# Performance work log

Measured on AMD Instinct MI355X. Metric: run time of the kernel, lower is better.

The kernel has to match this reference:

```python
import jax, jax.numpy as jnp
import numpy as np

B, N, D, H = 32, 128, 64, 128


def setup_inputs() -> dict:
    key = jax.random.key(0)
    ks = jax.random.split(key, 16)
    s = 0.05
    inp = {
        "x": jax.random.normal(ks[0], (B, N, D), dtype=jnp.float32),
        "masks": jax.random.randint(ks[1], (B, N), 0, 2, dtype=jnp.int32),
        # message_net: Linear(2D,H) -> ReLU -> Linear(H,H)
        "W1": jax.random.normal(ks[2], (2 * D, H), dtype=jnp.float32) * s,
        "b1": jax.random.normal(ks[3], (H,), dtype=jnp.float32) * s,
        "W2": jax.random.normal(ks[4], (H, H), dtype=jnp.float32) * s,
        "b2": jax.random.normal(ks[5], (H,), dtype=jnp.float32) * s,
        # attention_net: Linear(2D,H) -> ReLU -> Linear(H,1)
        "A1": jax.random.normal(ks[6], (2 * D, H), dtype=jnp.float32) * s,
        "ab1": jax.random.normal(ks[7], (H,), dtype=jnp.float32) * s,
        "A2": jax.random.normal(ks[8], (H, 1), dtype=jnp.float32) * s,
        "ab2": jax.random.normal(ks[9], (1,), dtype=jnp.float32) * s,
        # update_net: Linear(D+H,H) -> ReLU -> Linear(H,D)
        "U1": jax.random.normal(ks[10], (D + H, H), dtype=jnp.float32) * s,
        "ub1": jax.random.normal(ks[11], (H,), dtype=jnp.float32) * s,
        "U2": jax.random.normal(ks[12], (H, D), dtype=jnp.float32) * s,
        "ub2": jax.random.normal(ks[13], (D,), dtype=jnp.float32) * s,
    }
    return inp


def reference(x, masks, W1, b1, W2, b2, A1, ab1, A2, ab2, U1, ub1, U2, ub2):
    d = x.shape[-1]
    # pairs = cat([x_i, x_j]); Linear(pairs) == x_i @ W[:d] + x_j @ W[d:] + b
    # message MLP hidden: (B, N, N, H)
    h = jax.nn.relu(
        jnp.einsum("bid,dh->bih", x, W1[:d])[:, :, None, :]
        + jnp.einsum("bjd,dh->bjh", x, W1[d:])[:, None, :, :]
        + b1
    )
    messages = jnp.einsum("bijh,hk->bijk", h, W2) + b2  # (B, N, N, H)
    # attention MLP
    ha = jax.nn.relu(
        jnp.einsum("bid,dh->bih", x, A1[:d])[:, :, None, :]
        + jnp.einsum("bjd,dh->bjh", x, A1[d:])[:, None, :, :]
        + ab1
    )
    logits = jnp.einsum("bijh,h->bij", ha, A2[:, 0]) + ab2[0]  # (B, N, N)
    m = masks.astype(bool)[:, None, :]  # mask over j (source agents)
    logits = jnp.where(m, logits, -jnp.inf)
    attn = jax.nn.softmax(logits, axis=-1)
    attn = jnp.where(m, attn, 0.0)
    agg = jnp.einsum("bijh,bij->bih", messages, attn)  # (B, N, H)
    comb = jnp.concatenate([x, agg], axis=-1)  # (B, N, D+H)
    upd = jax.nn.relu(comb @ U1 + ub1) @ U2 + ub2  # (B, N, D)
    return x + upd
```

## Files before the change

### kernel.cpp

```cpp
#include <hip/hip_runtime.h>
#include <hip/hip_bf16.h>
#include <stdint.h>

#define NN 128
#define DD 64
#define HH 128

__device__ __forceinline__ float bflo(uint32_t u){ union{uint32_t u;float f;} c; c.u = u<<16; return c.f; }
__device__ __forceinline__ float bfhi(uint32_t u){ union{uint32_t u;float f;} c; c.u = u & 0xffff0000u; return c.f; }
__device__ __forceinline__ uint32_t packbf(float lo, float hi){
  __hip_bfloat16 a = __float2bfloat16(lo);
  __hip_bfloat16 b = __float2bfloat16(hi);
  uint16_t ua = *(uint16_t*)&a, ub = *(uint16_t*)&b;
  return (uint32_t)ua | ((uint32_t)ub<<16);
}

__global__ __launch_bounds__(128) void k1_proj(
    const float* __restrict__ x,
    const float* __restrict__ W1, const float* __restrict__ b1,
    const float* __restrict__ A1, const float* __restrict__ ab1,
    const float* __restrict__ W2, const float* __restrict__ b2,
    const float* __restrict__ U1, const float* __restrict__ ub1,
    float* __restrict__ Pm, float* __restrict__ Pa,
    uint32_t* __restrict__ Qmp, uint32_t* __restrict__ Qap,
    float* __restrict__ M, float* __restrict__ c0){
  const int bid = blockIdx.x;
  const int t = threadIdx.x;
  if(bid >= 512){
    int hb = bid - 512;
    if(hb < HH){
      float acc = 0.f;
      #pragma unroll 4
      for(int k=0;k<HH;k++) acc += W2[hb*HH+k] * U1[(DD+k)*HH+t];
      M[hb*HH+t] = acc;
    } else {
      float acc = ub1[t];
      #pragma unroll 4
      for(int k=0;k<HH;k++) acc += b2[k] * U1[(DD+k)*HH+t];
      c0[t] = acc;
    }
    return;
  }
  const int g = bid & 15, b = bid >> 4;
  const int jb = g*4;
  __shared__ float xs[8][64];
  __shared__ float qmS[8][128];
  __shared__ float qaS[8][128];
  {
    int r = t >> 4, d4 = (t & 15)*4;
    int gr = (r<4) ? (jb+r) : (jb + r - 4 + 64);
    *(float4*)&xs[r][d4] = *(const float4*)&x[(b*NN+gr)*DD + d4];
  }
  __syncthreads();
  float pm[8], qm[8], pa[8], qa[8];
  #pragma unroll
  for(int r=0;r<8;r++){ pm[r]=0.f;qm[r]=0.f;pa[r]=0.f;qa[r]=0.f; }
  for(int d0=0; d0<DD; d0+=4){
    float4 xr[8];
    #pragma unroll
    for(int r=0;r<8;r++) xr[r] = *(const float4*)&xs[r][d0];
    #pragma unroll
    for(int dd=0; dd<4; dd++){
      const int d = d0 + dd;
      float w1a = W1[d*HH + t];
      float w1b = W1[(DD+d)*HH + t];
      float a1a = A1[d*HH + t];
      float a1b = A1[(DD+d)*HH + t];
      #pragma unroll
      for(int r=0;r<8;r++){
        float xv = (&xr[r].x)[dd];
        pm[r] += xv*w1a; qm[r] += xv*w1b;
        pa[r] += xv*a1a; qa[r] += xv*a1b;
      }
    }
  }
  float b1v = b1[t], ab1v = ab1[t];
  #pragma unroll
  for(int r=0;r<8;r++){
    int gr = (r<4) ? (jb+r) : (jb + r - 4 + 64);
    Pm[(b*NN+gr)*HH + t] = pm[r] + b1v;
    Pa[(b*NN+gr)*HH + t] = pa[r] + ab1v;
    qmS[r][t] = qm[r];
    qaS[r][t] = qa[r];
  }
  __syncthreads();
  #pragma unroll
  for(int k=0;k<4;k++){
    int idx = t + k*128;
    int r = idx >> 6, hp = idx & 63;
    int gr = (r<4) ? (jb+r) : (jb + r - 4 + 64);
    Qmp[(b*NN+gr)*64 + hp] = packbf(qmS[r][hp], qmS[r][hp+64]);
    Qap[(b*NN+gr)*64 + hp] = packbf(qaS[r][hp], qaS[r][hp+64]);
  }
}

__global__ __launch_bounds__(256) void k2_fused(
    const float* __restrict__ Pa, const float* __restrict__ Pm,
    const uint32_t* __restrict__ Qap, const uint32_t* __restrict__ Qmp,
    const float* __restrict__ A2, const int* __restrict__ masks,
    const float* __restrict__ x, const float* __restrict__ M,
    const float* __restrict__ c0,
    const float* __restrict__ U1, const float* __restrict__ U2,
    const float* __restrict__ ub2, float* __restrict__ out){
  const int it = blockIdx.x;
  const int b  = blockIdx.y;
  const int t = threadIdx.x;
  const int wave = t>>6, lane = t&63;
  __shared__ uint32_t qbuf[NN*65];
  __shared__ float pS[8*HH];
  __shared__ float a2S[HH];
  __shared__ float atS[8*NN];
  __shared__ float xs[8][DD];
  {
    const uint32_t* src = Qap + (size_t)b*NN*64;
    #pragma unroll
    for(int k=0;k<8;k++){
      int idx4 = t + k*256;
      int j = idx4 >> 4, hp4 = (idx4 & 15)*4;
      uint4 v = *(const uint4*)&src[j*64 + hp4];
      uint32_t* d = &qbuf[j*65 + hp4];
      d[0]=v.x; d[1]=v.y; d[2]=v.z; d[3]=v.w;
    }
    int r = t>>5, h4 = (t&31)*4;
    *(float4*)&pS[r*HH + h4] = *(const float4*)&Pa[(b*NN + it*8 + r)*HH + h4];
    if(t < HH) a2S[t] = A2[t];
    if(t < 128){
      int xr = t >> 4, d4 = (t & 15)*4;
      *(float4*)&xs[xr][d4] = *(const float4*)&x[(b*NN + it*8 + xr)*DD + d4];
    }
  }
  __syncthreads();
  const int i0 = wave*2, i1 = i0+1;
  float a00=0.f,a01=0.f,a10=0.f,a11=0.f;
  for(int h0=0; h0<64; h0+=4){
    float4 p0a = *(const float4*)&pS[i0*HH + h0];
    float4 p0b = *(const float4*)&pS[i0*HH + 64 + h0];
    float4 p1a = *(const float4*)&pS[i1*HH + h0];
    float4 p1b = *(const float4*)&pS[i1*HH + 64 + h0];
    float4 a2a = *(const float4*)&a2S[h0];
    float4 a2b = *(const float4*)&a2S[64 + h0];
    #pragma unroll
    for(int dd=0; dd<4; dd++){
      uint32_t q0 = qbuf[lane*65 + h0 + dd];
      uint32_t q1 = qbuf[(lane+64)*65 + h0 + dd];
      float q0l=bflo(q0), q0h=bfhi(q0), q1l=bflo(q1), q1h=bfhi(q1);
      float pa0=(&p0a.x)[dd], pb0=(&p0b.x)[dd];
      float pa1=(&p1a.x)[dd], pb1=(&p1b.x)[dd];
      float aa=(&a2a.x)[dd],  ab=(&a2b.x)[dd];
      a00 += fmaxf(pa0+q0l,0.f)*aa; a00 += fmaxf(pb0+q0h,0.f)*ab;
      a01 += fmaxf(pa0+q1l,0.f)*aa; a01 += fmaxf(pb0+q1h,0.f)*ab;
      a10 += fmaxf(pa1+q0l,0.f)*aa; a10 += fmaxf(pb1+q0h,0.f)*ab;
      a11 += fmaxf(pa1+q1l,0.f)*aa; a11 += fmaxf(pb1+q1h,0.f)*ab;
    }
  }
  const int m0 = masks[b*NN + lane];
  const int m1 = masks[b*NN + 64 + lane];
  const float NEG = -3.0e38f;
  #pragma unroll
  for(int ii=0; ii<2; ii++){
    float x0 = ii ? a10 : a00, x1 = ii ? a11 : a01;
    int il = ii ? i1 : i0;
    float l0 = m0 ? x0 : NEG, l1 = m1 ? x1 : NEG;
    float v = fmaxf(l0, l1);
    for(int off=32; off>=1; off>>=1) v = fmaxf(v, __shfl_xor(v, off));
    float e0 = m0 ? __expf(x0 - v) : 0.f;
    float e1 = m1 ? __expf(x1 - v) : 0.f;
    float s = e0 + e1;
    for(int off=32; off>=1; off>>=1) s += __shfl_xor(s, off);
    float inv = (s > 0.f) ? (1.f/s) : 0.f;
    atS[il*NN + lane]      = e0*inv;
    atS[il*NN + 64 + lane] = e1*inv;
  }
  __syncthreads();
  {
    const uint32_t* src = Qmp + (size_t)b*NN*64;
    #pragma unroll
    for(int k=0;k<8;k++){
      int idx4 = t + k*256;
      int j = idx4 >> 4, hp4 = (idx4 & 15)*4;
      uint4 v = *(const uint4*)&src[j*64 + hp4];
      uint32_t* d = &qbuf[j*65 + hp4];
      d[0]=v.x; d[1]=v.y; d[2]=v.z; d[3]=v.w;
    }
    int r = t>>5, h4 = (t&31)*4;
    *(float4*)&pS[r*HH + h4] = *(const float4*)&Pm[(b*NN + it*8 + r)*HH + h4];
  }
  __syncthreads();
  float pm00 = pS[i0*HH + lane], pm01 = pS[i0*HH + 64 + lane];
  float pm10 = pS[i1*HH + lane], pm11 = pS[i1*HH + 64 + lane];
  float h00=0.f,h01=0.f,h10=0.f,h11=0.f;
  for(int j0=0; j0<NN; j0+=4){
    float4 at0 = *(const float4*)&atS[i0*NN + j0];
    float4 at1 = *(const float4*)&atS[i1*NN + j0];
    #pragma unroll
    for(int dd=0; dd<4; dd++){
      uint32_t qd = qbuf[(j0+dd)*65 + lane];
      float ql = bflo(qd), qh = bfhi(qd);
      float w0 = (&at0.x)[dd], w1 = (&at1.x)[dd];
      h00 += w0*fmaxf(pm00+ql,0.f);
      h01 += w0*fmaxf(pm01+qh,0.f);
      h10 += w1*fmaxf(pm10+ql,0.f);
      h11 += w1*fmaxf(pm11+qh,0.f);
    }
  }
  __syncthreads();
  pS[i0*HH + lane]      = h00;
  pS[i0*HH + 64 + lane] = h01;
  pS[i1*HH + lane]      = h10;
  pS[i1*HH + 64 + lane] = h11;
  __syncthreads();
  {
    const int c = t & 127, gg = t >> 7;
    float acc[4];
    #pragma unroll
    for(int r=0;r<4;r++) acc[r]=0.f;
    for(int d0=0; d0<DD; d0+=4){
      float u0 = U1[(d0+0)*HH + c];
      float u1 = U1[(d0+1)*HH + c];
      float u2 = U1[(d0+2)*HH + c];
      float u3 = U1[(d0+3)*HH + c];
      #pragma unroll
      for(int r=0;r<4;r++){
        float4 xv = *(const float4*)&xs[gg*4+r][d0];
        acc[r] += xv.x*u0 + xv.y*u1 + xv.z*u2 + xv.w*u3;
      }
    }
    for(int h0=0; h0<HH; h0+=4){
      float m0v = M[(h0+0)*HH + c];
      float m1v = M[(h0+1)*HH + c];
      float m2v = M[(h0+2)*HH + c];
      float m3v = M[(h0+3)*HH + c];
      #pragma unroll
      for(int r=0;r<4;r++){
        float4 hv = *(const float4*)&pS[(gg*4+r)*HH + h0];
        acc[r] += hv.x*m0v + hv.y*m1v + hv.z*m2v + hv.w*m3v;
      }
    }
    float cc = c0[c];
    #pragma unroll
    for(int r=0;r<4;r++) atS[(gg*4+r)*NN + c] = fmaxf(acc[r]+cc, 0.f);
  }
  __syncthreads();
  {
    const int dcol = t & 63, rg = t >> 6;
    float acc2[2];
    acc2[0]=0.f; acc2[1]=0.f;
    for(int ci=0; ci<HH; ci+=4){
      float u20 = U2[(ci+0)*DD + dcol];
      float u21 = U2[(ci+1)*DD + dcol];
      float u22 = U2[(ci+2)*DD + dcol];
      float u23 = U2[(ci+3)*DD + dcol];
      #pragma unroll
      for(int r=0;r<2;r++){
        float4 hv = *(const float4*)&atS[(rg*2+r)*NN + ci];
        acc2[r] += hv.x*u20 + hv.y*u21 + hv.z*u22 + hv.w*u23;
      }
    }
    float ub = ub2[dcol];
    #pragma unroll
    for(int r=0;r<2;r++){
      int grow = b*NN + it*8 + rg*2 + r;
      out[grow*DD + dcol] = xs[rg*2+r][dcol] + acc2[r] + ub;
    }
  }
}

extern "C" void kernel_launch(void* const* d_in, const int* in_sizes, int n_in,
                              void* d_out, int out_size, void* d_ws, size_t ws_size,
                              hipStream_t stream){
  const float* x   = (const float*)d_in[0];
  const int*   msk = (const int*)d_in[1];
  const float* W1  = (const float*)d_in[2];
  const float* b1  = (const float*)d_in[3];
  const float* W2  = (const float*)d_in[4];
  const float* b2  = (const float*)d_in[5];
  const float* A1  = (const float*)d_in[6];
  const float* ab1 = (const float*)d_in[7];
  const float* A2  = (const float*)d_in[8];
  const float* U1  = (const float*)d_in[10];
  const float* ub1 = (const float*)d_in[11];
  const float* U2  = (const float*)d_in[12];
  const float* ub2 = (const float*)d_in[13];
  float* out = (float*)d_out;

  char* w = (char*)d_ws;
  float*    Pm   = (float*)(w);
  float*    Pa   = (float*)(w + (2u<<20));
  uint32_t* Qmp  = (uint32_t*)(w + (4u<<20));
  uint32_t* Qap  = (uint32_t*)(w + (5u<<20));
  float*    M    = (float*)(w + (8u<<20));
  float*    c0   = (float*)(w + (8u<<20) + (64u<<10));

  hipLaunchKernelGGL(k1_proj, dim3(641), dim3(128), 0, stream,
                     x, W1, b1, A1, ab1, W2, b2, U1, ub1,
                     Pm, Pa, Qmp, Qap, M, c0);
  hipLaunchKernelGGL(k2_fused, dim3(16,32), dim3(256), 0, stream,
                     Pa, Pm, Qap, Qmp, A2, msk, x, M, c0, U1, U2, ub2, out);
}
```

Measured before the change: 117.1 us.

## Compact unmasked source agents and skip masked columns in fused attention kernel

Builds a compacted list of unmasked source indices per batch with a ballot and prefix popcount, then loads only those rows of the projected Q tensors into shared memory. The attention-logit loop skips the upper 64-column half when fewer than 64 sources remain, and the aggregation loop runs only over the compacted count. Masked sources get zero attention weight in the reference, so this removes work on them without changing the result. In exchange it adds two extra block barriers and some index bookkeeping, and the saving depends on the mask density (about half the agents are masked in the test inputs).

Measured after the change: 116.4 us. About the same (-0.6%).

```diff
diff --git a/kernel.cpp b/kernel.cpp
--- a/kernel.cpp
+++ b/kernel.cpp
@@ -111,16 +111,15 @@
   __shared__ float a2S[HH];
   __shared__ float atS[8*NN];
   __shared__ float xs[8][DD];
-  {
-    const uint32_t* src = Qap + (size_t)b*NN*64;
-    #pragma unroll
-    for(int k=0;k<8;k++){
-      int idx4 = t + k*256;
-      int j = idx4 >> 4, hp4 = (idx4 & 15)*4;
-      uint4 v = *(const uint4*)&src[j*64 + hp4];
-      uint32_t* d = &qbuf[j*65 + hp4];
-      d[0]=v.x; d[1]=v.y; d[2]=v.z; d[3]=v.w;
-    }
+  __shared__ unsigned long long balS[2];
+  __shared__ int jlS[NN];
+  int mym = 0;
+  if(t < 128) mym = masks[b*NN + t];
+  {
+    unsigned long long bal = __ballot(mym != 0);
+    if(wave < 2 && lane == 0) balS[wave] = bal;
+  }
+  {
     int r = t>>5, h4 = (t&31)*4;
     *(float4*)&pS[r*HH + h4] = *(const float4*)&Pa[(b*NN + it*8 + r)*HH + h4];
     if(t < HH) a2S[t] = A2[t];
@@ -130,7 +129,28 @@
     }
   }
   __syncthreads();
+  const int cnt0 = __popcll(balS[0]);
+  const int cnt  = cnt0 + __popcll(balS[1]);
+  const int cnt4 = (cnt + 3) & ~3;
+  if(t < 128 && mym){
+    unsigned long long bw = balS[wave];
+    int pos = __popcll(bw & ((1ull<<lane)-1)) + (wave ? cnt0 : 0);
+    jlS[pos] = t;
+  }
+  __syncthreads();
+  {
+    const uint32_t* src = Qap + (size_t)b*NN*64;
+    for(int idx4 = t; idx4 < cnt4*16; idx4 += 256){
+      int j = idx4 >> 4, hp4 = (idx4 & 15)*4;
+      uint4 v = make_uint4(0u,0u,0u,0u);
+      if(j < cnt) v = *(const uint4*)&src[jlS[j]*64 + hp4];
+      uint32_t* d = &qbuf[j*65 + hp4];
+      d[0]=v.x; d[1]=v.y; d[2]=v.z; d[3]=v.w;
+    }
+  }
+  __syncthreads();
   const int i0 = wave*2, i1 = i0+1;
+  const bool hasHi = (cnt > 64);
   float a00=0.f,a01=0.f,a10=0.f,a11=0.f;
   for(int h0=0; h0<64; h0+=4){
     float4 p0a = *(const float4*)&pS[i0*HH + h0];
@@ -142,29 +162,38 @@
     #pragma unroll
     for(int dd=0; dd<4; dd++){
       uint32_t q0 = qbuf[lane*65 + h0 + dd];
-      uint32_t q1 = qbuf[(lane+64)*65 + h0 + dd];
-      float q0l=bflo(q0), q0h=bfhi(q0), q1l=bflo(q1), q1h=bfhi(q1);
+      float q0l=bflo(q0), q0h=bfhi(q0);
       float pa0=(&p0a.x)[dd], pb0=(&p0b.x)[dd];
       float pa1=(&p1a.x)[dd], pb1=(&p1b.x)[dd];
       float aa=(&a2a.x)[dd],  ab=(&a2b.x)[dd];
       a00 += fmaxf(pa0+q0l,0.f)*aa; a00 += fmaxf(pb0+q0h,0.f)*ab;
-      a01 += fmaxf(pa0+q1l,0.f)*aa; a01 += fmaxf(pb0+q1h,0.f)*ab;
       a10 += fmaxf(pa1+q0l,0.f)*aa; a10 += fmaxf(pb1+q0h,0.f)*ab;
-      a11 += fmaxf(pa1+q1l,0.f)*aa; a11 += fmaxf(pb1+q1h,0.f)*ab;
-    }
-  }
-  const int m0 = masks[b*NN + lane];
-  const int m1 = masks[b*NN + 64 + lane];
+    }
+    if(hasHi){
+      #pragma unroll
+      for(int dd=0; dd<4; dd++){
+        uint32_t q1 = qbuf[(lane+64)*65 + h0 + dd];
+        float q1l=bflo(q1), q1h=bfhi(q1);
+        float pa0=(&p0a.x)[dd], pb0=(&p0b.x)[dd];
+        float pa1=(&p1a.x)[dd], pb1=(&p1b.x)[dd];
+        float aa=(&a2a.x)[dd],  ab=(&a2b.x)[dd];
+        a01 += fmaxf(pa0+q1l,0.f)*aa; a01 += fmaxf(pb0+q1h,0.f)*ab;
+        a11 += fmaxf(pa1+q1l,0.f)*aa; a11 += fmaxf(pb1+q1h,0.f)*ab;
+      }
+    }
+  }
+  const bool v0c = (lane < cnt);
+  const bool v1c = (lane + 64 < cnt);
   const float NEG = -3.0e38f;
   #pragma unroll
   for(int ii=0; ii<2; ii++){
     float x0 = ii ? a10 : a00, x1 = ii ? a11 : a01;
     int il = ii ? i1 : i0;
-    float l0 = m0 ? x0 : NEG, l1 = m1 ? x1 : NEG;
+    float l0 = v0c ? x0 : NEG, l1 = v1c ? x1 : NEG;
     float v = fmaxf(l0, l1);
     for(int off=32; off>=1; off>>=1) v = fmaxf(v, __shfl_xor(v, off));
-    float e0 = m0 ? __expf(x0 - v) : 0.f;
-    float e1 = m1 ? __expf(x1 - v) : 0.f;
+    float e0 = v0c ? __expf(x0 - v) : 0.f;
+    float e1 = v1c ? __expf(x1 - v) : 0.f;
     float s = e0 + e1;
     for(int off=32; off>=1; off>>=1) s += __shfl_xor(s, off);
     float inv = (s > 0.f) ? (1.f/s) : 0.f;
@@ -174,11 +203,10 @@
   __syncthreads();
   {
     const uint32_t* src = Qmp + (size_t)b*NN*64;
-    #pragma unroll
-    for(int k=0;k<8;k++){
-      int idx4 = t + k*256;
+    for(int idx4 = t; idx4 < cnt4*16; idx4 += 256){
       int j = idx4 >> 4, hp4 = (idx4 & 15)*4;
-      uint4 v = *(const uint4*)&src[j*64 + hp4];
+      uint4 v = make_uint4(0u,0u,0u,0u);
+      if(j < cnt) v = *(const uint4*)&src[jlS[j]*64 + hp4];
       uint32_t* d = &qbuf[j*65 + hp4];
       d[0]=v.x; d[1]=v.y; d[2]=v.z; d[3]=v.w;
     }
@@ -189,7 +217,7 @@
   float pm00 = pS[i0*HH + lane], pm01 = pS[i0*HH + 64 + lane];
   float pm10 = pS[i1*HH + lane], pm11 = pS[i1*HH + 64 + lane];
   float h00=0.f,h01=0.f,h10=0.f,h11=0.f;
-  for(int j0=0; j0<NN; j0+=4){
+  for(int j0=0; j0<cnt4; j0+=4){
     float4 at0 = *(const float4*)&atS[i0*NN + j0];
     float4 at1 = *(const float4*)&atS[i1*NN + j0];
     #pragma unroll
```
